# Optimization experiments

Measured on AMD Instinct MI355X. Metric: run time of the kernel, lower is better.

The kernel has to match this reference:

```python
import jax, jax.numpy as jnp
import numpy as np

N = 100_000      # nodes
E = 800_000      # edges per edge type
T = 3            # num_edge_types - 1 relation-specific convs
D_IN = 128
D_OUT = 128


def setup_inputs() -> dict:
    key = jax.random.key(0)
    k1, k2, k3, k4 = jax.random.split(key, 4)
    x = jax.random.normal(k1, (N, D_IN), dtype=jnp.float32)
    edges = jax.random.randint(k2, (T, 2, E), 0, N, dtype=jnp.int32)
    W = jax.random.normal(k3, (T, D_IN, D_OUT), dtype=jnp.float32) * (1.0 / np.sqrt(D_IN))
    b = jax.random.normal(k4, (T, D_OUT), dtype=jnp.float32) * 0.02
    return {"x": x, "edges": edges, "W": W, "b": b}


def _gcn_conv(x, ei, W, b):
    """PyG GCNConv: add self-loops, symmetric D^-1/2 (A+I) D^-1/2 norm, XW, +b."""
    n = x.shape[0]
    xw = x @ W                                   # [N, D_OUT]
    loop = jnp.arange(n, dtype=ei.dtype)
    src = jnp.concatenate([ei[0], loop])         # [E+N]
    dst = jnp.concatenate([ei[1], loop])         # [E+N]
    deg = jax.ops.segment_sum(jnp.ones(src.shape[0], xw.dtype), dst, num_segments=n)
    dis = jnp.where(deg > 0, jax.lax.rsqrt(jnp.maximum(deg, 1e-12)), 0.0)
    norm = dis[src] * dis[dst]                   # [E+N]
    msg = xw[src] * norm[:, None]                # gather-transform: [E+N, D_OUT]
    out = jax.ops.segment_sum(msg, dst, num_segments=n)  # scatter-add back to nodes
    return out + b


def reference(x, edges, W, b):
    # Sum of per-edge-type GCN convolutions into a shared output buffer.
    out = jnp.zeros((x.shape[0], W.shape[-1]), dtype=x.dtype)
    for i in range(edges.shape[0]):              # small fixed relation loop
        out = out + _gcn_conv(x, edges[i], W[i], b[i])
    return out
```

## Files before the change

### kernel.cpp

```cpp
#include <hip/hip_runtime.h>

#define NN 100000
#define EE 800000
#define TT 3
#define D  128
#define NB 391
#define CAPB 7168
#define CHUNK 4096
#define LSTRIDE 392

typedef unsigned short bf16_t;

typedef __bf16 bf16x8_t __attribute__((ext_vector_type(8)));
typedef float  f32x4_t  __attribute__((ext_vector_type(4)));

union ABFrag { bf16x8_t v; uint4 q; };

__device__ __forceinline__ bf16_t f2bf(float f) {
    unsigned u = __float_as_uint(f);
    u += 0x7fff + ((u >> 16) & 1);
    return (bf16_t)(u >> 16);
}
__device__ __forceinline__ float bf_lo(unsigned p) { return __uint_as_float(p << 16); }
__device__ __forceinline__ float bf_hi(unsigned p) { return __uint_as_float(p & 0xFFFF0000u); }

__global__ void quant_kernel(const float* __restrict__ x, bf16_t* __restrict__ xq) {
    int i = (blockIdx.x * 256 + threadIdx.x) * 4;
    if (i >= NN * D) return;
    float4 f = *(const float4*)(x + i);
    uint2 p;
    p.x = (unsigned)f2bf(f.x) | ((unsigned)f2bf(f.y) << 16);
    p.y = (unsigned)f2bf(f.z) | ((unsigned)f2bf(f.w) << 16);
    *(uint2*)(xq + i) = p;
}

__global__ void wconv_kernel(const float* __restrict__ W, bf16_t* __restrict__ WT) {
    int t = blockIdx.y, n = blockIdx.x, k = threadIdx.x;
    WT[((size_t)t * D + n) * D + k] = f2bf(W[((size_t)t * D + k) * D + n]);
}

__global__ __launch_bounds__(512, 8) void bin_kernel(const int* __restrict__ edges,
                                                     int* __restrict__ bcnt,
                                                     unsigned* __restrict__ bin) {
    __shared__ int hist[NB];
    __shared__ int lbase[NB];
    __shared__ int gbase[NB];
    __shared__ int scn[512];
    __shared__ unsigned srec[CHUNK];
    __shared__ unsigned stgt[CHUNK];
    int tid = threadIdx.x;
    int t = blockIdx.y;
    int f0 = blockIdx.x * CHUNK;
    const int* sb = edges + (size_t)t * 2 * EE;
    const int* db = sb + EE;

    for (int i = tid; i < NB; i += 512) hist[i] = 0;
    __syncthreads();

    int4 s4[2], d4[2];
    int rnk[8];
    bool have[2];
#pragma unroll
    for (int j = 0; j < 2; ++j) {
        int e = f0 + ((j * 512 + tid) << 2);
        have[j] = (e < EE);
        if (have[j]) { s4[j] = *(const int4*)(sb + e); d4[j] = *(const int4*)(db + e); }
    }
#pragma unroll
    for (int j = 0; j < 2; ++j) {
        if (have[j]) {
            rnk[j * 4 + 0] = atomicAdd(&hist[d4[j].x >> 8], 1);
            rnk[j * 4 + 1] = atomicAdd(&hist[d4[j].y >> 8], 1);
            rnk[j * 4 + 2] = atomicAdd(&hist[d4[j].z >> 8], 1);
            rnk[j * 4 + 3] = atomicAdd(&hist[d4[j].w >> 8], 1);
        }
    }
    __syncthreads();

    int hv = (tid < NB) ? hist[tid] : 0;
    scn[tid] = hv;
    __syncthreads();
    for (int off = 1; off < 512; off <<= 1) {
        int u = 0;
        if (tid >= off) u = scn[tid - off];
        __syncthreads();
        if (tid >= off) scn[tid] += u;
        __syncthreads();
    }
    if (tid < NB) {
        lbase[tid] = scn[tid] - hv;
        gbase[tid] = (hv > 0) ? atomicAdd(&bcnt[tid], hv) : 0;
    }
    __syncthreads();

#pragma unroll
    for (int j = 0; j < 2; ++j) {
        if (have[j]) {
            int ss[4] = {s4[j].x, s4[j].y, s4[j].z, s4[j].w};
            int dd[4] = {d4[j].x, d4[j].y, d4[j].z, d4[j].w};
#pragma unroll
            for (int k = 0; k < 4; ++k) {
                int bkt = dd[k] >> 8;
                int r = rnk[j * 4 + k];
                int pos = lbase[bkt] + r;
                int rel = gbase[bkt] + r;
                srec[pos] = ((unsigned)(dd[k] & 255) << 19) | ((unsigned)t << 17) | (unsigned)ss[k];
                stgt[pos] = (rel < CAPB) ? (unsigned)(bkt * CAPB + rel) : 0xFFFFFFFFu;
            }
        }
    }
    __syncthreads();

    int nval = EE - f0; if (nval > CHUNK) nval = CHUNK;
    for (int i = tid; i < nval; i += 512) {
        unsigned tg = stgt[i];
        if (tg != 0xFFFFFFFFu) bin[tg] = srec[i];
    }
}

#define MAXR 14
__global__ __launch_bounds__(512) void sort_kernel(const int* __restrict__ bcnt,
                                                   unsigned* __restrict__ bin,
                                                   float* __restrict__ dis3,
                                                   int* __restrict__ cnts3,
                                                   int* __restrict__ nodeoff) {
    __shared__ int cnt[768];
    __shared__ int tot[256];
    int tid = threadIdx.x;
    int b = blockIdx.x;
    int c = bcnt[b]; if (c > CAPB) c = CAPB;
    unsigned* reg = bin + (size_t)b * CAPB;

    for (int i = tid; i < 768; i += 512) cnt[i] = 0;
    __syncthreads();

    unsigned ur[MAXR];
    int rr[MAXR];
    bool vld[MAXR];
#pragma unroll
    for (int k = 0; k < MAXR; ++k) {
        int i = tid + k * 512;
        vld[k] = (i < c);
        unsigned u = vld[k] ? reg[i] : 0u;
        ur[k] = u;
        int bi = (int)(u >> 19) * 3 + (int)((u >> 17) & 3);
        rr[k] = vld[k] ? atomicAdd(&cnt[bi], 1) : 0;
    }
    __syncthreads();

    int d0 = 0, d1 = 0, d2 = 0;
    if (tid < 256) {
        d0 = cnt[tid * 3]; d1 = cnt[tid * 3 + 1]; d2 = cnt[tid * 3 + 2];
        tot[tid] = d0 + d1 + d2;
    }
    __syncthreads();
    for (int off = 1; off < 256; off <<= 1) {
        int v = 0;
        if (tid < 256 && tid >= off) v = tot[tid - off];
        __syncthreads();
        if (tid < 256 && tid >= off) tot[tid] += v;
        __syncthreads();
    }
    if (tid < 256) {
        int excl = tot[tid] - (d0 + d1 + d2);
        int gnode = b * 256 + tid;
        if (gnode < NN) {
            nodeoff[gnode] = b * CAPB + excl;
            cnts3[gnode]   = d0 | (d1 << 8) | (d2 << 16);
            dis3[gnode]            = rsqrtf((float)d0 + 1.f);
            dis3[NN + gnode]       = rsqrtf((float)d1 + 1.f);
            dis3[2 * NN + gnode]   = rsqrtf((float)d2 + 1.f);
        }
        cnt[tid * 3]     = excl;
        cnt[tid * 3 + 1] = excl + d0;
        cnt[tid * 3 + 2] = excl + d0 + d1;
    }
    __syncthreads();
#pragma unroll
    for (int k = 0; k < MAXR; ++k) {
        if (vld[k]) {
            unsigned u = ur[k];
            int bi = (int)(u >> 19) * 3 + (int)((u >> 17) & 3);
            reg[cnt[bi] + rr[k]] = u & 0x1FFFFu;
        }
    }
}


#define ISSUE(UX, WA, J0)                                                          \
    {                                                                              \
        const int _j0 = (J0);                                                      \
        _Pragma("unroll")                                                          \
        for (int k = 0; k < 8; ++k) {                                              \
            int sxk = __builtin_amdgcn_readlane(vsrc, _j0 + k);                    \
            int wbk = __builtin_amdgcn_readlane(wbits, _j0 + k);                   \
            WA[k] = __int_as_float(wbk);                                           \
            UX[k] = *(const unsigned*)(xq + (size_t)sxk * D + (lane << 1));        \
        }                                                                          \
    }

#define CONSUME(UX, WA, J0)                                                        \
    {                                                                              \
        const int _j0 = (J0);                                                      \
        _Pragma("unroll")                                                          \
        for (int k = 0; k < 8; ++k) {                                              \
            int idxk = _j0 + k;                                                    \
            float wk = WA[k];                                                      \
            unsigned u = UX[k];                                                    \
            float xl = bf_lo(u), xh = bf_hi(u);                                    \
            if (idxk < b1S)      { a00 += wk * xl; a01 += wk * xh; }               \
            else if (idxk < b2S) { a10 += wk * xl; a11 += wk * xh; }               \
            else                 { a20 += wk * xl; a21 += wk * xh; }               \
        }                                                                          \
    }

__global__ __launch_bounds__(1024, 8) void fused_kernel(const bf16_t* __restrict__ xq,
                                                        const float* __restrict__ dis3,
                                                        const int* __restrict__ cnts3,
                                                        const int* __restrict__ nodeoff,
                                                        const unsigned* __restrict__ recs,
                                                        const bf16_t* __restrict__ WT,
                                                        const float* __restrict__ bias,
                                                        float* __restrict__ out) {
    __shared__ __attribute__((aligned(16))) ushort ylds[16 * LSTRIDE];
    int tid  = threadIdx.x;
    int lane = tid & 63;
    int wave = tid >> 6;
    int n0 = blockIdx.x * 16;
    int n  = n0 + wave;

    unsigned su = *(const unsigned*)(xq + (size_t)n * D + (lane << 1));
    float xs0 = bf_lo(su), xs1 = bf_hi(su);

    float dn0 = dis3[n], dn1 = dis3[NN + n], dn2 = dis3[2 * NN + n];
    int pk = cnts3[n];
    int d0 = pk & 255, d1 = (pk >> 8) & 255, d2 = (pk >> 16) & 255;
    int s0 = nodeoff[n];

    int b1S = __builtin_amdgcn_readfirstlane(d0);
    int b2S = __builtin_amdgcn_readfirstlane(d0 + d1);
    int cT  = d0 + d1 + d2; if (cT > 64) cT = 64;
    int cS  = __builtin_amdgcn_readfirstlane(cT);

    unsigned u = recs[s0 + lane];
    int tl = (lane < b1S) ? 0 : (lane < b2S) ? 1 : 2;
    int vsrc = (int)(u & 0x1FFFFu);
    if (vsrc >= NN) vsrc = 0;
    float ws = 0.0f;
    if (lane < cS) ws = dis3[tl * NN + vsrc];
    int wbits = __float_as_int(ws);

    float a00 = dn0 * xs0, a01 = dn0 * xs1;
    float a10 = dn1 * xs0, a11 = dn1 * xs1;
    float a20 = dn2 * xs0, a21 = dn2 * xs1;

    unsigned uxA[8], uxB[8];
    float wA[8], wB[8];

    if (cS > 0) {
        int nb = (cS + 7) >> 3;
        ISSUE(uxA, wA, 0)
        int blk = 0;
        while (true) {
            if (blk + 1 < nb) ISSUE(uxB, wB, (blk + 1) * 8)
            CONSUME(uxA, wA, blk * 8)
            if (++blk >= nb) break;
            if (blk + 1 < nb) ISSUE(uxA, wA, (blk + 1) * 8)
            CONSUME(uxB, wB, blk * 8)
            if (++blk >= nb) break;
        }
    }

    {
        a00 *= dn0; a01 *= dn0; a10 *= dn1; a11 *= dn1; a20 *= dn2; a21 *= dn2;
        ushort* yw = ylds + wave * LSTRIDE + (lane << 1);
        *(unsigned*)(yw)         = (unsigned)f2bf(a00) | ((unsigned)f2bf(a01) << 16);
        *(unsigned*)(yw + D)     = (unsigned)f2bf(a10) | ((unsigned)f2bf(a11) << 16);
        *(unsigned*)(yw + 2 * D) = (unsigned)f2bf(a20) | ((unsigned)f2bf(a21) << 16);
    }
    __syncthreads();

    if (wave < 8) {
        int quad = lane >> 4;
        int lid  = lane & 15;
        int col  = wave * 16 + lid;
        f32x4_t acc = {0.f, 0.f, 0.f, 0.f};
        const ushort* yr = ylds + lid * LSTRIDE;
#pragma unroll
        for (int t = 0; t < TT; ++t) {
            const bf16_t* wn = WT + ((size_t)t * D + col) * D;
#pragma unroll
            for (int s = 0; s < 4; ++s) {
                ABFrag av, bv;
                av.q = *(const uint4*)(yr + t * D + s * 32 + quad * 8);
                bv.q = *(const uint4*)(wn + s * 32 + quad * 8);
                acc = __builtin_amdgcn_mfma_f32_16x16x32_bf16(av.v, bv.v, acc, 0, 0, 0);
            }
        }
        float bc = bias[col] + bias[D + col] + bias[2 * D + col];
#pragma unroll
        for (int r = 0; r < 4; ++r)
            out[(size_t)(n0 + quad * 4 + r) * D + col] = acc[r] + bc;
    }
}

extern "C" void kernel_launch(void* const* d_in, const int* in_sizes, int n_in,
                              void* d_out, int out_size, void* d_ws, size_t ws_size,
                              hipStream_t stream) {
    const float* x     = (const float*)d_in[0];
    const int*   edges = (const int*)d_in[1];
    const float* W     = (const float*)d_in[2];
    const float* b     = (const float*)d_in[3];
    float*       out   = (float*)d_out;

    char* w = (char*)d_ws;
    bf16_t*   xq      = (bf16_t*)w;
    unsigned* bin     = (unsigned*)(w + (size_t)NN * D * 2);
    float*    dis3    = (float*)((char*)bin + (size_t)NB * CAPB * 4);
    int*      cnts3   = (int*)((char*)dis3 + (size_t)3 * NN * 4);
    int*      nodeoff = cnts3 + NN;
    bf16_t*   WT      = (bf16_t*)(nodeoff + NN);
    int*      bcnt    = (int*)((char*)WT + (size_t)TT * D * D * 2);

    hipMemsetAsync(bcnt, 0, (size_t)NB * sizeof(int), stream);

    quant_kernel<<<(NN * D / 4 + 255) / 256, 256, 0, stream>>>(x, xq);
    {
        dim3 g(D, TT);
        wconv_kernel<<<g, D, 0, stream>>>(W, WT);
    }

    {
        dim3 g((EE + CHUNK - 1) / CHUNK, TT);
        bin_kernel<<<g, 512, 0, stream>>>(edges, bcnt, bin);
    }

    sort_kernel<<<NB, 512, 0, stream>>>(bcnt, bin, dis3, cnts3, nodeoff);

    fused_kernel<<<NN / 16, 1024, 0, stream>>>(xq, dis3, cnts3, nodeoff, bin, WT, b, out);
}
```

Baseline: 308.9 us.

## Pre-bake quantized neighbor weights into edge records and double bin chunk size

Adds a weightize pass after sorting. It replaces each record's edge-type bits with a 15-bit fixed-point encoding of the source node's degree normalisation. The fused kernel then decodes the weight from the record and no longer does a per-lane gather from dis3 before aggregation. The bin kernel now processes 8192 edges per block with a lower occupancy hint. The cost is an extra kernel launch and a pass over all records, plus quantisation error in the edge weights.

```diff
diff --git a/kernel.cpp b/kernel.cpp
--- a/kernel.cpp
+++ b/kernel.cpp
@@ -6,8 +6,9 @@
 #define D  128
 #define NB 391
 #define CAPB 7168
-#define CHUNK 4096
+#define CHUNK 8192
 #define LSTRIDE 392
+#define ENC 32767.0f
 
 typedef unsigned short bf16_t;
 
@@ -39,7 +40,7 @@
     WT[((size_t)t * D + n) * D + k] = f2bf(W[((size_t)t * D + k) * D + n]);
 }
 
-__global__ __launch_bounds__(512, 8) void bin_kernel(const int* __restrict__ edges,
+__global__ __launch_bounds__(512, 4) void bin_kernel(const int* __restrict__ edges,
                                                      int* __restrict__ bcnt,
                                                      unsigned* __restrict__ bin) {
     __shared__ int hist[NB];
@@ -57,17 +58,17 @@
     for (int i = tid; i < NB; i += 512) hist[i] = 0;
     __syncthreads();
 
-    int4 s4[2], d4[2];
-    int rnk[8];
-    bool have[2];
-#pragma unroll
-    for (int j = 0; j < 2; ++j) {
+    int4 s4[4], d4[4];
+    int rnk[16];
+    bool have[4];
+#pragma unroll
+    for (int j = 0; j < 4; ++j) {
         int e = f0 + ((j * 512 + tid) << 2);
         have[j] = (e < EE);
         if (have[j]) { s4[j] = *(const int4*)(sb + e); d4[j] = *(const int4*)(db + e); }
     }
 #pragma unroll
-    for (int j = 0; j < 2; ++j) {
+    for (int j = 0; j < 4; ++j) {
         if (have[j]) {
             rnk[j * 4 + 0] = atomicAdd(&hist[d4[j].x >> 8], 1);
             rnk[j * 4 + 1] = atomicAdd(&hist[d4[j].y >> 8], 1);
@@ -94,7 +95,7 @@
     __syncthreads();
 
 #pragma unroll
-    for (int j = 0; j < 2; ++j) {
+    for (int j = 0; j < 4; ++j) {
         if (have[j]) {
             int ss[4] = {s4[j].x, s4[j].y, s4[j].z, s4[j].w};
             int dd[4] = {d4[j].x, d4[j].y, d4[j].z, d4[j].w};
@@ -181,31 +182,45 @@
         if (vld[k]) {
             unsigned u = ur[k];
             int bi = (int)(u >> 19) * 3 + (int)((u >> 17) & 3);
-            reg[cnt[bi] + rr[k]] = u & 0x1FFFFu;
-        }
-    }
-}
-
-
-#define ISSUE(UX, WA, J0)                                                          \
+            reg[cnt[bi] + rr[k]] = u & 0x7FFFFu;
+        }
+    }
+}
+
+__global__ __launch_bounds__(512) void weightize_kernel(const int* __restrict__ bcnt,
+                                                        const float* __restrict__ dis3,
+                                                        unsigned* __restrict__ bin) {
+    int b = blockIdx.x;
+    int c = bcnt[b]; if (c > CAPB) c = CAPB;
+    unsigned* reg = bin + (size_t)b * CAPB;
+    for (int i = threadIdx.x; i < c; i += 512) {
+        unsigned u = reg[i];
+        unsigned src = u & 0x1FFFFu;
+        unsigned t = (u >> 17) & 3u;
+        float w = dis3[t * NN + src];
+        reg[i] = ((unsigned)(w * ENC + 0.5f) << 17) | src;
+    }
+}
+
+
+#define ISSUE(UX, SA, J0)                                                          \
     {                                                                              \
         const int _j0 = (J0);                                                      \
         _Pragma("unroll")                                                          \
         for (int k = 0; k < 8; ++k) {                                              \
-            int sxk = __builtin_amdgcn_readlane(vsrc, _j0 + k);                    \
-            int wbk = __builtin_amdgcn_readlane(wbits, _j0 + k);                   \
-            WA[k] = __int_as_float(wbk);                                           \
+            SA[k] = __builtin_amdgcn_readlane((int)uw, _j0 + k);                   \
+            int sxk = SA[k] & 0x1FFFF;                                             \
             UX[k] = *(const unsigned*)(xq + (size_t)sxk * D + (lane << 1));        \
         }                                                                          \
     }
 
-#define CONSUME(UX, WA, J0)                                                        \
+#define CONSUME(UX, SA, J0)                                                        \
     {                                                                              \
         const int _j0 = (J0);                                                      \
         _Pragma("unroll")                                                          \
         for (int k = 0; k < 8; ++k) {                                              \
             int idxk = _j0 + k;                                                    \
-            float wk = WA[k];                                                      \
+            float wk = (float)(((unsigned)SA[k]) >> 17);                           \
             unsigned u = UX[k];                                                    \
             float xl = bf_lo(u), xh = bf_hi(u);                                    \
             if (idxk < b1S)      { a00 += wk * xl; a01 += wk * xh; }               \
@@ -242,37 +257,33 @@
     int cT  = d0 + d1 + d2; if (cT > 64) cT = 64;
     int cS  = __builtin_amdgcn_readfirstlane(cT);
 
-    unsigned u = recs[s0 + lane];
-    int tl = (lane < b1S) ? 0 : (lane < b2S) ? 1 : 2;
-    int vsrc = (int)(u & 0x1FFFFu);
-    if (vsrc >= NN) vsrc = 0;
-    float ws = 0.0f;
-    if (lane < cS) ws = dis3[tl * NN + vsrc];
-    int wbits = __float_as_int(ws);
-
-    float a00 = dn0 * xs0, a01 = dn0 * xs1;
-    float a10 = dn1 * xs0, a11 = dn1 * xs1;
-    float a20 = dn2 * xs0, a21 = dn2 * xs1;
+    unsigned uraw = recs[s0 + lane];
+    unsigned uw = (lane < cS) ? uraw : 0u;
+
+    float a00 = dn0 * ENC * xs0, a01 = dn0 * ENC * xs1;
+    float a10 = dn1 * ENC * xs0, a11 = dn1 * ENC * xs1;
+    float a20 = dn2 * ENC * xs0, a21 = dn2 * ENC * xs1;
 
     unsigned uxA[8], uxB[8];
-    float wA[8], wB[8];
+    int sA[8], sB[8];
 
     if (cS > 0) {
         int nb = (cS + 7) >> 3;
-        ISSUE(uxA, wA, 0)
+        ISSUE(uxA, sA, 0)
         int blk = 0;
         while (true) {
-            if (blk + 1 < nb) ISSUE(uxB, wB, (blk + 1) * 8)
-            CONSUME(uxA, wA, blk * 8)
+            if (blk + 1 < nb) ISSUE(uxB, sB, (blk + 1) * 8)
+            CONSUME(uxA, sA, blk * 8)
             if (++blk >= nb) break;
-            if (blk + 1 < nb) ISSUE(uxA, wA, (blk + 1) * 8)
-            CONSUME(uxB, wB, blk * 8)
+            if (blk + 1 < nb) ISSUE(uxA, sA, (blk + 1) * 8)
+            CONSUME(uxB, sB, blk * 8)
             if (++blk >= nb) break;
         }
     }
 
     {
-        a00 *= dn0; a01 *= dn0; a10 *= dn1; a11 *= dn1; a20 *= dn2; a21 *= dn2;
+        float f0 = dn0 * (1.0f / ENC), f1 = dn1 * (1.0f / ENC), f2 = dn2 * (1.0f / ENC);
+        a00 *= f0; a01 *= f0; a10 *= f1; a11 *= f1; a20 *= f2; a21 *= f2;
         ushort* yw = ylds + wave * LSTRIDE + (lane << 1);
         *(unsigned*)(yw)         = (unsigned)f2bf(a00) | ((unsigned)f2bf(a01) << 16);
         *(unsigned*)(yw + D)     = (unsigned)f2bf(a10) | ((unsigned)f2bf(a11) << 16);
@@ -337,5 +348,7 @@
 
     sort_kernel<<<NB, 512, 0, stream>>>(bcnt, bin, dis3, cnts3, nodeoff);
 
+    weightize_kernel<<<NB, 512, 0, stream>>>(bcnt, dis3, bin);
+
     fused_kernel<<<NN / 16, 1024, 0, stream>>>(xq, dis3, cnts3, nodeoff, bin, WT, b, out);
 }
```

Result: no change. 313.2 us (+1.4%).
